# Optimization experiments

Hardware: AMD Instinct MI355X
Metric: run time of the kernel (lower is better)

The kernel has to match this reference:

```python
import jax, jax.numpy as jnp
import numpy as np

B, S, D = 4, 2048, 1024

def setup_inputs() -> dict:
    key = jax.random.key(0)
    k1, k2, k3, k4 = jax.random.split(key, 4)
    output = jax.random.normal(k1, (B, S, D), dtype=jnp.float32)
    # nn.Linear(dim, dim, bias=False): y = x @ W.T ; store W as [D, D]
    scale = 1.0 / np.sqrt(D)
    w_q = jax.random.uniform(k2, (D, D), dtype=jnp.float32, minval=-scale, maxval=scale)
    w_k = jax.random.uniform(k3, (D, D), dtype=jnp.float32, minval=-scale, maxval=scale)
    w_v = jax.random.uniform(k4, (D, D), dtype=jnp.float32, minval=-scale, maxval=scale)
    return {"output": output, "w_q": w_q, "w_k": w_k, "w_v": w_v}

def reference(output, w_q, w_k, w_v):
    # projections: x @ W.T (torch Linear convention)
    q = jnp.einsum('bsd,ed->bse', output, w_q)
    k = jnp.einsum('bsd,ed->bse', output, w_k)
    v = jnp.einsum('bsd,ed->bse', output, w_v)
    scores = jnp.einsum('bqd,bkd->bqk', q, k)      # unscaled, no mask
    attn = jax.nn.softmax(scores, axis=-1)
    return jnp.einsum('bqk,bkd->bqd', attn, v)
```

## Files before the change

### kernel.cpp

```cpp
#include <hip/hip_runtime.h>
#include <stdint.h>


typedef __attribute__((ext_vector_type(8))) _Float16 f16x8;
typedef __attribute__((ext_vector_type(4))) float f32x4;
typedef __attribute__((ext_vector_type(4))) unsigned short u16x4;

__device__ inline unsigned short f2h(float f) {
    union { _Float16 h; unsigned short u; } x;
    x.h = (_Float16)f;
    return x.u;
}
__device__ inline float h2f(unsigned short u) {
    union { unsigned short u; _Float16 h; } x;
    x.u = u;
    return (float)x.h;
}

__device__ inline void async16(const unsigned short* g, unsigned short* l) {
    __builtin_amdgcn_global_load_lds(
        (__attribute__((address_space(1))) void*)g,
        (__attribute__((address_space(3))) void*)l, 16, 0, 0);
}

template <int MODE, int BN>
__global__ __launch_bounds__(512)
void gemm512(const unsigned short* __restrict__ A,
             const unsigned short* __restrict__ B,
             void* __restrict__ C, void* __restrict__ C2,
             int K, int ldA, int ldB, int ldC,
             long sAz, long sBz, long sCz)
{
    static_assert(BN == 128, "pipeline is derived for BN=128");
    constexpr int NT = BN / 32;
    constexpr int BI = BN / 64;
    constexpr int TILE = 256 * 64 + BN * 64;
    __shared__ __align__(16) unsigned short smem[2 * TILE];

    const int tid  = threadIdx.x;
    const int lane = tid & 63;
    const int wave = tid >> 6;
    const int wr   = wave >> 1, wc = wave & 1;
    const int quad = lane >> 4, lrow = lane & 15;
    const int bm   = blockIdx.x, bn = blockIdx.y, z = blockIdx.z;

    const unsigned short* Az = A + (long)z * sAz;
    const unsigned short* Bz = B + (long)z * sBz;

    const unsigned short* gA[4];
    const unsigned short* gB[BI];
#pragma unroll
    for (int i = 0; i < 4; ++i) {
        const int l = tid + 512 * i;
        const int r = l >> 3;
        const int c = (l & 7) ^ (r & 7);
        gA[i] = Az + (long)(bm * 256 + r) * ldA + c * 8;
    }
#pragma unroll
    for (int i = 0; i < BI; ++i) {
        const int l = tid + 512 * i;
        const int r = l >> 3;
        const int c = (l & 7) ^ (r & 7);
        gB[i] = Bz + (long)(bn * BN + r) * ldB + c * 8;
    }

    f32x4 acc[4][NT];
#pragma unroll
    for (int i = 0; i < 4; ++i)
#pragma unroll
        for (int j = 0; j < NT; ++j)
            acc[i][j] = f32x4{0.f, 0.f, 0.f, 0.f};

    const int fr = lrow & 7;
    const int ntiles = K >> 6;

#pragma unroll
    for (int i = 0; i < 4; ++i)
        async16(gA[i], &smem[(tid + 512 * i) * 8]);
#pragma unroll
    for (int i = 0; i < BI; ++i)
        async16(gB[i], &smem[256 * 64 + (tid + 512 * i) * 8]);
#pragma unroll
    for (int i = 0; i < 4; ++i) {
        async16(gA[i] + 64, &smem[TILE + (tid + 512 * i) * 8]);
        gA[i] += 128;
    }
#pragma unroll
    for (int i = 0; i < BI; ++i) gB[i] += 64;

    asm volatile("s_waitcnt vmcnt(4)" ::: "memory");
    __builtin_amdgcn_s_barrier();

    for (int t = 0; t < ntiles; ++t) {
        const unsigned short* cA = smem + (t & 1) * TILE;
        const unsigned short* cB = cA + 256 * 64;
        unsigned short* nxt  = smem + ((t + 1) & 1) * TILE;
        unsigned short* cur  = smem + (t & 1) * TILE;

        f16x8 af[4][2], b0f[2][2];
#pragma unroll
        for (int ks = 0; ks < 2; ++ks) {
            const int pc = (((ks << 2) + quad) ^ fr) * 8;
#pragma unroll
            for (int mt = 0; mt < 4; ++mt)
                af[mt][ks] = *(const f16x8*)&cA[(wr * 64 + mt * 16 + lrow) * 64 + pc];
#pragma unroll
            for (int n = 0; n < 2; ++n)
                b0f[n][ks] = *(const f16x8*)&cB[(wc * (BN / 2) + n * 16 + lrow) * 64 + pc];
        }
        if (t + 1 < ntiles) {
#pragma unroll
            for (int i = 0; i < BI; ++i) {
                async16(gB[i], &nxt[256 * 64 + (tid + 512 * i) * 8]);
                gB[i] += 64;
            }
        }
        __builtin_amdgcn_s_barrier();
        asm volatile("s_waitcnt lgkmcnt(0)");
        __builtin_amdgcn_s_setprio(1);
#pragma unroll
        for (int mt = 0; mt < 4; ++mt)
#pragma unroll
            for (int n = 0; n < 2; ++n)
#pragma unroll
                for (int ks = 0; ks < 2; ++ks)
                    acc[mt][n] = __builtin_amdgcn_mfma_f32_16x16x32_f16(
                        af[mt][ks], b0f[n][ks], acc[mt][n], 0, 0, 0);
        __builtin_amdgcn_s_setprio(0);
        __builtin_amdgcn_s_barrier();

        f16x8 b1f[2][2];
#pragma unroll
        for (int ks = 0; ks < 2; ++ks) {
            const int pc = (((ks << 2) + quad) ^ fr) * 8;
#pragma unroll
            for (int n = 0; n < 2; ++n)
                b1f[n][ks] = *(const f16x8*)&cB[(wc * (BN / 2) + (2 + n) * 16 + lrow) * 64 + pc];
        }
        if (t + 2 < ntiles) {
#pragma unroll
            for (int i = 0; i < 4; ++i) {
                async16(gA[i], &cur[(tid + 512 * i) * 8]);
                gA[i] += 64;
            }
        }
        __builtin_amdgcn_s_barrier();
        asm volatile("s_waitcnt lgkmcnt(0)");
        __builtin_amdgcn_s_setprio(1);
#pragma unroll
        for (int mt = 0; mt < 4; ++mt)
#pragma unroll
            for (int n = 0; n < 2; ++n)
#pragma unroll
                for (int ks = 0; ks < 2; ++ks)
                    acc[mt][2 + n] = __builtin_amdgcn_mfma_f32_16x16x32_f16(
                        af[mt][ks], b1f[n][ks], acc[mt][2 + n], 0, 0, 0);
        __builtin_amdgcn_s_setprio(0);
        if (t + 2 < ntiles)
            asm volatile("s_waitcnt vmcnt(4)" ::: "memory");
        else if (t + 1 < ntiles)
            asm volatile("s_waitcnt vmcnt(0)" ::: "memory");
        __builtin_amdgcn_s_barrier();
    }

    const int col_base = bn * BN + wc * (BN / 2);

    if (MODE != 0 || z < 2) {
        const int row_base = bm * 256 + wr * 64;
        const long zC = (long)z * sCz;
#pragma unroll
        for (int mt = 0; mt < 4; ++mt)
#pragma unroll
            for (int nt = 0; nt < NT; ++nt)
#pragma unroll
                for (int r = 0; r < 4; ++r) {
                    const int row = row_base + mt * 16 + quad * 4 + r;
                    const int col = col_base + nt * 16 + lrow;
                    if (MODE == 2)
                        ((float*)C)[zC + (long)row * ldC + col] = acc[mt][nt][r];
                    else
                        ((unsigned short*)C)[zC + (long)row * ldC + col] =
                            f2h(acc[mt][nt][r]);
                }
    } else {
        unsigned short* T = smem;
#pragma unroll
        for (int p = 0; p < 4; ++p) {
            __syncthreads();
            if (wr == p) {
#pragma unroll
                for (int mt = 0; mt < 4; ++mt)
#pragma unroll
                    for (int nt = 0; nt < NT; ++nt) {
                        const int row_l = mt * 16 + quad * 4;
                        const int col_l = wc * 64 + nt * 16 + lrow;
                        u16x4 pk = {f2h(acc[mt][nt][0]), f2h(acc[mt][nt][1]),
                                    f2h(acc[mt][nt][2]), f2h(acc[mt][nt][3])};
                        *(u16x4*)&T[col_l * 72 + row_l] = pk;
                    }
            }
            __syncthreads();
            const int c  = tid >> 2;
            const int j0 = (tid & 3) * 16;
            const int tok0 = bm * 256 + p * 64;
            const int bb = tok0 >> 11;
            const int s0 = (tok0 & 2047) + j0;
            unsigned short* dst = (unsigned short*)C2 + (long)bb * 2097152 +
                                  (long)(bn * 128 + c) * 2048 + s0;
            const unsigned short* srcT = &T[c * 72 + j0];
            *(f16x8*)dst = *(const f16x8*)srcT;
            *(f16x8*)(dst + 8) = *(const f16x8*)(srcT + 8);
        }
    }
}

__global__ __launch_bounds__(256)
void cvt_all(const float* __restrict__ x, const float* __restrict__ w0,
             const float* __restrict__ w1, const float* __restrict__ w2,
             unsigned short* __restrict__ xh, unsigned short* __restrict__ wh)
{
    const int bid = blockIdx.x;
    const float* s;
    unsigned short* d;
    long i;
    if (bid < 4096) {
        s = x; d = xh;
        i = ((long)bid * 256 + threadIdx.x) * 8;
    } else {
        const int wid = bid - 4096;
        const int w = wid >> 9;
        s = (w == 0) ? w0 : (w == 1) ? w1 : w2;
        d = wh + (long)w * 1048576;
        i = ((long)(wid & 511) * 256 + threadIdx.x) * 8;
    }
    f32x4 a = *(const f32x4*)(s + i);
    f32x4 b = *(const f32x4*)(s + i + 4);
    union { unsigned short u[8]; f16x8 v; } t;
#pragma unroll
    for (int j = 0; j < 4; ++j) { t.u[j] = f2h(a[j]); t.u[4 + j] = f2h(b[j]); }
    *(f16x8*)(d + i) = t.v;
}

__global__ __launch_bounds__(256)
void softmax16(unsigned short* __restrict__ sc)
{
    const long row = blockIdx.x;
    unsigned short* srow = sc + row * 2048;
    const int tid = threadIdx.x;

    union { u16x4 p[2]; unsigned short u[8]; } in;
    in.p[0] = *(const u16x4*)(srow + tid * 8);
    in.p[1] = *(const u16x4*)(srow + tid * 8 + 4);
    float v[8];
#pragma unroll
    for (int i = 0; i < 8; ++i) v[i] = h2f(in.u[i]);

    float m = v[0];
#pragma unroll
    for (int i = 1; i < 8; ++i) m = fmaxf(m, v[i]);
#pragma unroll
    for (int off = 32; off; off >>= 1) m = fmaxf(m, __shfl_xor(m, off));

    __shared__ float redm[4], reds[4];
    if ((tid & 63) == 0) redm[tid >> 6] = m;
    __syncthreads();
    m = fmaxf(fmaxf(redm[0], redm[1]), fmaxf(redm[2], redm[3]));

    float s = 0.f;
#pragma unroll
    for (int i = 0; i < 8; ++i) { v[i] = __expf(v[i] - m); s += v[i]; }
#pragma unroll
    for (int off = 32; off; off >>= 1) s += __shfl_xor(s, off);
    if ((tid & 63) == 0) reds[tid >> 6] = s;
    __syncthreads();
    s = reds[0] + reds[1] + reds[2] + reds[3];

    const float inv = 1.f / s;
    union { unsigned short u[8]; f16x8 w; } t;
#pragma unroll
    for (int i = 0; i < 8; ++i) t.u[i] = f2h(v[i] * inv);
    *(f16x8*)(srow + tid * 8) = t.w;
}

extern "C" void kernel_launch(void* const* d_in, const int* in_sizes, int n_in,
                              void* d_out, int out_size, void* d_ws, size_t ws_size,
                              hipStream_t stream)
{
    const float* x  = (const float*)d_in[0];
    const float* wq = (const float*)d_in[1];
    const float* wk = (const float*)d_in[2];
    const float* wv = (const float*)d_in[3];
    float* out = (float*)d_out;

    char* base = (char*)d_ws;
    const bool batched = (ws_size >= 88080384UL);

    unsigned short* xh = (unsigned short*)base;
    unsigned short* wh = (unsigned short*)(base + 16777216);
    unsigned short* sc = (unsigned short*)base;
    unsigned short* q  = (unsigned short*)(base + (batched ? 33554432 : 23068672));
    unsigned short* k  = q + 8388608;
    unsigned short* vt = k + 8388608;

    cvt_all<<<5632, 256, 0, stream>>>(x, wq, wk, wv, xh, wh);

    gemm512<0, 128><<<dim3(32, 8, 3), 512, 0, stream>>>(
        xh, wh, q, vt, 1024, 1024, 1024, 1024, 0L, 1048576L, 8388608L);

    if (batched) {
        gemm512<1, 128><<<dim3(8, 16, 4), 512, 0, stream>>>(
            q, k, sc, nullptr, 1024, 1024, 1024, 2048,
            2097152L, 2097152L, 4194304L);
        softmax16<<<8192, 256, 0, stream>>>(sc);
        gemm512<2, 128><<<dim3(8, 8, 4), 512, 0, stream>>>(
            sc, vt, out, nullptr, 2048, 2048, 2048, 1024,
            4194304L, 2097152L, 2097152L);
    } else {
        for (int b = 0; b < 4; ++b) {
            gemm512<1, 128><<<dim3(8, 16, 1), 512, 0, stream>>>(
                q + (long)b * 2097152, k + (long)b * 2097152, sc, nullptr,
                1024, 1024, 1024, 2048, 0L, 0L, 0L);
            softmax16<<<2048, 256, 0, stream>>>(sc);
            gemm512<2, 128><<<dim3(8, 8, 1), 512, 0, stream>>>(
                sc, vt + (long)b * 2097152, out + (long)b * 2097152, nullptr,
                2048, 2048, 2048, 1024, 0L, 0L, 0L);
        }
    }
}
```

Measured before the change: 250.3 us.

## Switch GEMM to 256x256 block tiles with four-phase quadrant pipeline

Replaces the 256x128 GEMM tile with a 256x256 tile split into four 128x128 quadrants. Waves are now arranged 2x4, and the A/B half-tiles are prefetched in a four-stage ping-pong schedule that interleaves loads with MFMA phases. Each block does more arithmetic per byte loaded, which cuts global and LDS traffic, and the grid sizes are halved along N. The cost is more accumulator registers per thread (128 floats), larger LDS use (128KB), fewer blocks for the smaller GEMMs, and a more intricate vmcnt/barrier schedule.

```diff
diff --git a/kernel.cpp b/kernel.cpp
--- a/kernel.cpp
+++ b/kernel.cpp
@@ -23,97 +23,95 @@
         (__attribute__((address_space(3))) void*)l, 16, 0, 0);
 }
 
-template <int MODE, int BN>
+template <int MODE>
 __global__ __launch_bounds__(512)
-void gemm512(const unsigned short* __restrict__ A,
+void gemm256(const unsigned short* __restrict__ A,
              const unsigned short* __restrict__ B,
              void* __restrict__ C, void* __restrict__ C2,
              int K, int ldA, int ldB, int ldC,
              long sAz, long sBz, long sCz)
 {
-    static_assert(BN == 128, "pipeline is derived for BN=128");
-    constexpr int NT = BN / 32;
-    constexpr int BI = BN / 64;
-    constexpr int TILE = 256 * 64 + BN * 64;
-    __shared__ __align__(16) unsigned short smem[2 * TILE];
+    __shared__ __align__(16) unsigned short smem[65536];
 
     const int tid  = threadIdx.x;
     const int lane = tid & 63;
     const int wave = tid >> 6;
-    const int wr   = wave >> 1, wc = wave & 1;
+    const int wr   = wave >> 2;
+    const int wc   = wave & 3;
     const int quad = lane >> 4, lrow = lane & 15;
-    const int bm   = blockIdx.x, bn = blockIdx.y, z = blockIdx.z;
+    const int bm = blockIdx.x, bn = blockIdx.y, z = blockIdx.z;
 
     const unsigned short* Az = A + (long)z * sAz;
     const unsigned short* Bz = B + (long)z * sBz;
 
-    const unsigned short* gA[4];
-    const unsigned short* gB[BI];
-#pragma unroll
-    for (int i = 0; i < 4; ++i) {
-        const int l = tid + 512 * i;
-        const int r = l >> 3;
-        const int c = (l & 7) ^ (r & 7);
-        gA[i] = Az + (long)(bm * 256 + r) * ldA + c * 8;
-    }
-#pragma unroll
-    for (int i = 0; i < BI; ++i) {
-        const int l = tid + 512 * i;
-        const int r = l >> 3;
-        const int c = (l & 7) ^ (r & 7);
-        gB[i] = Bz + (long)(bn * BN + r) * ldB + c * 8;
-    }
-
-    f32x4 acc[4][NT];
-#pragma unroll
-    for (int i = 0; i < 4; ++i)
-#pragma unroll
-        for (int j = 0; j < NT; ++j)
-            acc[i][j] = f32x4{0.f, 0.f, 0.f, 0.f};
-
-    const int fr = lrow & 7;
+    const unsigned short* gA[2][2];
+    const unsigned short* gB[2][2];
+#pragma unroll
+    for (int h = 0; h < 2; ++h)
+#pragma unroll
+        for (int i = 0; i < 2; ++i) {
+            const int l = tid + 512 * i;
+            const int r = l >> 3;
+            const int c = (l & 7) ^ (r & 7);
+            gA[h][i] = Az + (long)(bm * 256 + h * 128 + r) * ldA + c * 8;
+            gB[h][i] = Bz + (long)(bn * 256 + h * 128 + r) * ldB + c * 8;
+        }
+
+    f32x4 acc[2][2][4][2];
+#pragma unroll
+    for (int a = 0; a < 2; ++a)
+#pragma unroll
+        for (int b = 0; b < 2; ++b)
+#pragma unroll
+            for (int m = 0; m < 4; ++m)
+#pragma unroll
+                for (int n = 0; n < 2; ++n)
+                    acc[a][b][m][n] = f32x4{0.f, 0.f, 0.f, 0.f};
+
+    const int fr  = lrow & 7;
+    const int pc0 = (quad ^ fr) * 8;
+    const int pc1 = ((4 + quad) ^ fr) * 8;
     const int ntiles = K >> 6;
 
-#pragma unroll
-    for (int i = 0; i < 4; ++i)
-        async16(gA[i], &smem[(tid + 512 * i) * 8]);
-#pragma unroll
-    for (int i = 0; i < BI; ++i)
-        async16(gB[i], &smem[256 * 64 + (tid + 512 * i) * 8]);
-#pragma unroll
-    for (int i = 0; i < 4; ++i) {
-        async16(gA[i] + 64, &smem[TILE + (tid + 512 * i) * 8]);
-        gA[i] += 128;
-    }
-#pragma unroll
-    for (int i = 0; i < BI; ++i) gB[i] += 64;
+    async16(gA[1][0], smem + 8192 + tid * 8);
+    async16(gA[1][1], smem + 8192 + (tid + 512) * 8);
+    async16(gB[0][0], smem + 16384 + tid * 8);
+    async16(gB[0][1], smem + 16384 + (tid + 512) * 8);
+    async16(gA[0][0], smem + tid * 8);
+    async16(gA[0][1], smem + (tid + 512) * 8);
+    async16(gB[1][0], smem + 24576 + tid * 8);
+    async16(gB[1][1], smem + 24576 + (tid + 512) * 8);
+#pragma unroll
+    for (int h = 0; h < 2; ++h)
+#pragma unroll
+        for (int i = 0; i < 2; ++i) { gA[h][i] += 64; gB[h][i] += 64; }
 
     asm volatile("s_waitcnt vmcnt(4)" ::: "memory");
     __builtin_amdgcn_s_barrier();
 
+    f16x8 af[2][4][2], bf[2][2];
+
     for (int t = 0; t < ntiles; ++t) {
-        const unsigned short* cA = smem + (t & 1) * TILE;
-        const unsigned short* cB = cA + 256 * 64;
-        unsigned short* nxt  = smem + ((t + 1) & 1) * TILE;
-        unsigned short* cur  = smem + (t & 1) * TILE;
-
-        f16x8 af[4][2], b0f[2][2];
-#pragma unroll
-        for (int ks = 0; ks < 2; ++ks) {
-            const int pc = (((ks << 2) + quad) ^ fr) * 8;
-#pragma unroll
-            for (int mt = 0; mt < 4; ++mt)
-                af[mt][ks] = *(const f16x8*)&cA[(wr * 64 + mt * 16 + lrow) * 64 + pc];
-#pragma unroll
-            for (int n = 0; n < 2; ++n)
-                b0f[n][ks] = *(const f16x8*)&cB[(wc * (BN / 2) + n * 16 + lrow) * 64 + pc];
-        }
-        if (t + 1 < ntiles) {
-#pragma unroll
-            for (int i = 0; i < BI; ++i) {
-                async16(gB[i], &nxt[256 * 64 + (tid + 512 * i) * 8]);
-                gB[i] += 64;
-            }
+        const unsigned short* sb = smem + (t & 1) * 32768;
+        unsigned short*       nb = smem + ((t + 1) & 1) * 32768;
+        const bool pf = (t + 1 < ntiles);
+
+#pragma unroll
+        for (int mt = 0; mt < 4; ++mt) {
+            const int ro = 8192 + (wr * 64 + mt * 16 + lrow) * 64;
+            af[1][mt][0] = *(const f16x8*)&sb[ro + pc0];
+            af[1][mt][1] = *(const f16x8*)&sb[ro + pc1];
+        }
+#pragma unroll
+        for (int n = 0; n < 2; ++n) {
+            const int ro = 16384 + (wc * 32 + n * 16 + lrow) * 64;
+            bf[n][0] = *(const f16x8*)&sb[ro + pc0];
+            bf[n][1] = *(const f16x8*)&sb[ro + pc1];
+        }
+        if (pf) {
+            async16(gA[1][0], nb + 8192 + tid * 8);
+            async16(gA[1][1], nb + 8192 + (tid + 512) * 8);
+            gA[1][0] += 64; gA[1][1] += 64;
         }
         __builtin_amdgcn_s_barrier();
         asm volatile("s_waitcnt lgkmcnt(0)");
@@ -124,25 +122,23 @@
             for (int n = 0; n < 2; ++n)
 #pragma unroll
                 for (int ks = 0; ks < 2; ++ks)
-                    acc[mt][n] = __builtin_amdgcn_mfma_f32_16x16x32_f16(
-                        af[mt][ks], b0f[n][ks], acc[mt][n], 0, 0, 0);
+                    acc[1][0][mt][n] = __builtin_amdgcn_mfma_f32_16x16x32_f16(
+                        af[1][mt][ks], bf[n][ks], acc[1][0][mt][n], 0, 0, 0);
         __builtin_amdgcn_s_setprio(0);
-        __builtin_amdgcn_s_barrier();
-
-        f16x8 b1f[2][2];
-#pragma unroll
-        for (int ks = 0; ks < 2; ++ks) {
-            const int pc = (((ks << 2) + quad) ^ fr) * 8;
-#pragma unroll
-            for (int n = 0; n < 2; ++n)
-                b1f[n][ks] = *(const f16x8*)&cB[(wc * (BN / 2) + (2 + n) * 16 + lrow) * 64 + pc];
-        }
-        if (t + 2 < ntiles) {
-#pragma unroll
-            for (int i = 0; i < 4; ++i) {
-                async16(gA[i], &cur[(tid + 512 * i) * 8]);
-                gA[i] += 64;
-            }
+        if (pf) asm volatile("s_waitcnt vmcnt(4)" ::: "memory");
+        else    asm volatile("s_waitcnt vmcnt(2)" ::: "memory");
+        __builtin_amdgcn_s_barrier();
+
+#pragma unroll
+        for (int mt = 0; mt < 4; ++mt) {
+            const int ro = (wr * 64 + mt * 16 + lrow) * 64;
+            af[0][mt][0] = *(const f16x8*)&sb[ro + pc0];
+            af[0][mt][1] = *(const f16x8*)&sb[ro + pc1];
+        }
+        if (pf) {
+            async16(gB[0][0], nb + 16384 + tid * 8);
+            async16(gB[0][1], nb + 16384 + (tid + 512) * 8);
+            gB[0][0] += 64; gB[0][1] += 64;
         }
         __builtin_amdgcn_s_barrier();
         asm volatile("s_waitcnt lgkmcnt(0)");
@@ -153,63 +149,115 @@
             for (int n = 0; n < 2; ++n)
 #pragma unroll
                 for (int ks = 0; ks < 2; ++ks)
-                    acc[mt][2 + n] = __builtin_amdgcn_mfma_f32_16x16x32_f16(
-                        af[mt][ks], b1f[n][ks], acc[mt][2 + n], 0, 0, 0);
+                    acc[0][0][mt][n] = __builtin_amdgcn_mfma_f32_16x16x32_f16(
+                        af[0][mt][ks], bf[n][ks], acc[0][0][mt][n], 0, 0, 0);
         __builtin_amdgcn_s_setprio(0);
-        if (t + 2 < ntiles)
-            asm volatile("s_waitcnt vmcnt(4)" ::: "memory");
-        else if (t + 1 < ntiles)
-            asm volatile("s_waitcnt vmcnt(0)" ::: "memory");
+        if (pf) asm volatile("s_waitcnt vmcnt(4)" ::: "memory");
+        else    asm volatile("s_waitcnt vmcnt(0)" ::: "memory");
+        __builtin_amdgcn_s_barrier();
+
+#pragma unroll
+        for (int n = 0; n < 2; ++n) {
+            const int ro = 24576 + (wc * 32 + n * 16 + lrow) * 64;
+            bf[n][0] = *(const f16x8*)&sb[ro + pc0];
+            bf[n][1] = *(const f16x8*)&sb[ro + pc1];
+        }
+        if (pf) {
+            async16(gA[0][0], nb + tid * 8);
+            async16(gA[0][1], nb + (tid + 512) * 8);
+            gA[0][0] += 64; gA[0][1] += 64;
+        }
+        __builtin_amdgcn_s_barrier();
+        asm volatile("s_waitcnt lgkmcnt(0)");
+        __builtin_amdgcn_s_setprio(1);
+#pragma unroll
+        for (int mt = 0; mt < 4; ++mt)
+#pragma unroll
+            for (int n = 0; n < 2; ++n)
+#pragma unroll
+                for (int ks = 0; ks < 2; ++ks)
+                    acc[1][1][mt][n] = __builtin_amdgcn_mfma_f32_16x16x32_f16(
+                        af[1][mt][ks], bf[n][ks], acc[1][1][mt][n], 0, 0, 0);
+        __builtin_amdgcn_s_setprio(0);
+        __builtin_amdgcn_s_barrier();
+
+        if (pf) {
+            async16(gB[1][0], nb + 24576 + tid * 8);
+            async16(gB[1][1], nb + 24576 + (tid + 512) * 8);
+            gB[1][0] += 64; gB[1][1] += 64;
+        }
+        __builtin_amdgcn_s_setprio(1);
+#pragma unroll
+        for (int mt = 0; mt < 4; ++mt)
+#pragma unroll
+            for (int n = 0; n < 2; ++n)
+#pragma unroll
+                for (int ks = 0; ks < 2; ++ks)
+                    acc[0][1][mt][n] = __builtin_amdgcn_mfma_f32_16x16x32_f16(
+                        af[0][mt][ks], bf[n][ks], acc[0][1][mt][n], 0, 0, 0);
+        __builtin_amdgcn_s_setprio(0);
+        if (pf) asm volatile("s_waitcnt vmcnt(4)" ::: "memory");
         __builtin_amdgcn_s_barrier();
     }
 
-    const int col_base = bn * BN + wc * (BN / 2);
-
     if (MODE != 0 || z < 2) {
-        const int row_base = bm * 256 + wr * 64;
         const long zC = (long)z * sCz;
 #pragma unroll
-        for (int mt = 0; mt < 4; ++mt)
-#pragma unroll
-            for (int nt = 0; nt < NT; ++nt)
-#pragma unroll
-                for (int r = 0; r < 4; ++r) {
-                    const int row = row_base + mt * 16 + quad * 4 + r;
-                    const int col = col_base + nt * 16 + lrow;
-                    if (MODE == 2)
-                        ((float*)C)[zC + (long)row * ldC + col] = acc[mt][nt][r];
-                    else
-                        ((unsigned short*)C)[zC + (long)row * ldC + col] =
-                            f2h(acc[mt][nt][r]);
-                }
+        for (int mh = 0; mh < 2; ++mh)
+#pragma unroll
+            for (int nh = 0; nh < 2; ++nh)
+#pragma unroll
+                for (int mt = 0; mt < 4; ++mt)
+#pragma unroll
+                    for (int n = 0; n < 2; ++n)
+#pragma unroll
+                        for (int r = 0; r < 4; ++r) {
+                            const int row = bm * 256 + mh * 128 + wr * 64 +
+                                            mt * 16 + quad * 4 + r;
+                            const int col = bn * 256 + nh * 128 + wc * 32 +
+                                            n * 16 + lrow;
+                            if (MODE == 2)
+                                ((float*)C)[zC + (long)row * ldC + col] =
+                                    acc[mh][nh][mt][n][r];
+                            else
+                                ((unsigned short*)C)[zC + (long)row * ldC + col] =
+                                    f2h(acc[mh][nh][mt][n][r]);
+                        }
     } else {
         unsigned short* T = smem;
 #pragma unroll
         for (int p = 0; p < 4; ++p) {
             __syncthreads();
-            if (wr == p) {
+            if (wr == (p & 1)) {
+                const int mh = p >> 1;
 #pragma unroll
                 for (int mt = 0; mt < 4; ++mt)
 #pragma unroll
-                    for (int nt = 0; nt < NT; ++nt) {
-                        const int row_l = mt * 16 + quad * 4;
-                        const int col_l = wc * 64 + nt * 16 + lrow;
-                        u16x4 pk = {f2h(acc[mt][nt][0]), f2h(acc[mt][nt][1]),
-                                    f2h(acc[mt][nt][2]), f2h(acc[mt][nt][3])};
-                        *(u16x4*)&T[col_l * 72 + row_l] = pk;
-                    }
+                    for (int nh = 0; nh < 2; ++nh)
+#pragma unroll
+                        for (int n = 0; n < 2; ++n) {
+                            const int row_l = mt * 16 + quad * 4;
+                            const int col_l = nh * 128 + wc * 32 + n * 16 + lrow;
+                            u16x4 pk = {f2h(acc[mh][nh][mt][n][0]),
+                                        f2h(acc[mh][nh][mt][n][1]),
+                                        f2h(acc[mh][nh][mt][n][2]),
+                                        f2h(acc[mh][nh][mt][n][3])};
+                            *(u16x4*)&T[col_l * 72 + row_l] = pk;
+                        }
             }
             __syncthreads();
-            const int c  = tid >> 2;
-            const int j0 = (tid & 3) * 16;
+            const int c  = tid >> 1;
+            const int j0 = (tid & 1) * 32;
             const int tok0 = bm * 256 + p * 64;
             const int bb = tok0 >> 11;
             const int s0 = (tok0 & 2047) + j0;
             unsigned short* dst = (unsigned short*)C2 + (long)bb * 2097152 +
-                                  (long)(bn * 128 + c) * 2048 + s0;
+                                  (long)(bn * 256 + c) * 2048 + s0;
             const unsigned short* srcT = &T[c * 72 + j0];
-            *(f16x8*)dst = *(const f16x8*)srcT;
-            *(f16x8*)(dst + 8) = *(const f16x8*)(srcT + 8);
+            *(f16x8*)dst        = *(const f16x8*)srcT;
+            *(f16x8*)(dst + 8)  = *(const f16x8*)(srcT + 8);
+            *(f16x8*)(dst + 16) = *(const f16x8*)(srcT + 16);
+            *(f16x8*)(dst + 24) = *(const f16x8*)(srcT + 24);
         }
     }
 }
@@ -304,24 +352,24 @@
 
     cvt_all<<<5632, 256, 0, stream>>>(x, wq, wk, wv, xh, wh);
 
-    gemm512<0, 128><<<dim3(32, 8, 3), 512, 0, stream>>>(
+    gemm256<0><<<dim3(32, 4, 3), 512, 0, stream>>>(
         xh, wh, q, vt, 1024, 1024, 1024, 1024, 0L, 1048576L, 8388608L);
 
     if (batched) {
-        gemm512<1, 128><<<dim3(8, 16, 4), 512, 0, stream>>>(
+        gemm256<1><<<dim3(8, 8, 4), 512, 0, stream>>>(
             q, k, sc, nullptr, 1024, 1024, 1024, 2048,
             2097152L, 2097152L, 4194304L);
         softmax16<<<8192, 256, 0, stream>>>(sc);
-        gemm512<2, 128><<<dim3(8, 8, 4), 512, 0, stream>>>(
+        gemm256<2><<<dim3(8, 4, 4), 512, 0, stream>>>(
             sc, vt, out, nullptr, 2048, 2048, 2048, 1024,
             4194304L, 2097152L, 2097152L);
     } else {
         for (int b = 0; b < 4; ++b) {
-            gemm512<1, 128><<<dim3(8, 16, 1), 512, 0, stream>>>(
+            gemm256<1><<<dim3(8, 8, 1), 512, 0, stream>>>(
                 q + (long)b * 2097152, k + (long)b * 2097152, sc, nullptr,
                 1024, 1024, 1024, 2048, 0L, 0L, 0L);
             softmax16<<<2048, 256, 0, stream>>>(sc);
-            gemm512<2, 128><<<dim3(8, 8, 1), 512, 0, stream>>>(
+            gemm256<2><<<dim3(8, 4, 1), 512, 0, stream>>>(
                 sc, vt + (long)b * 2097152, out + (long)b * 2097152, nullptr,
                 2048, 2048, 2048, 1024, 0L, 0L, 0L);
         }
```

After: 266.0 us. +6.3%, slower.
